# Optimization experiments

Hardware: AMD Instinct MI355X
Metric: run time of the kernel (lower is better)

The kernel has to match this reference:

```python
import jax, jax.numpy as jnp
import numpy as np

N = 100000
E = 3200000
D = 128


def setup_inputs() -> dict:
    key = jax.random.key(0)
    k1, k2, k3, k4 = jax.random.split(key, 4)
    x = jax.random.normal(k1, (N, D), dtype=jnp.float32)
    edge_index = jax.random.randint(k2, (2, E), 0, N, dtype=jnp.int64)
    W1 = jax.random.normal(k3, (D, 16), dtype=jnp.float32) * (1.0 / np.sqrt(D))
    b1 = jnp.zeros((16,), dtype=jnp.float32)
    W2 = jax.random.normal(k4, (16, 2), dtype=jnp.float32) * (1.0 / np.sqrt(16))
    b2 = jnp.zeros((2,), dtype=jnp.float32)
    return {"x": x, "edge_index": edge_index, "W1": W1, "b1": b1, "W2": W2, "b2": b2}


def _gcn_conv(h, src, dst, norm, W, b):
    # transform first (out_dim <= in_dim), then normalized scatter-add aggregation
    h = h @ W                                   # [N, out]
    msg = h[src] * norm[:, None]                # [E+N, out] gathered messages
    agg = jax.ops.segment_sum(msg, dst, num_segments=N)
    return agg + b


def reference(x, edge_index, W1, b1, W2, b2):
    loops = jnp.arange(N, dtype=edge_index.dtype)
    src = jnp.concatenate([edge_index[0], loops])   # row (message source)
    dst = jnp.concatenate([edge_index[1], loops])   # col (aggregation target)
    # symmetric GCN normalization: deg over dst, norm = d^-1/2[src] * d^-1/2[dst]
    deg = jax.ops.segment_sum(jnp.ones_like(src, dtype=x.dtype), dst, num_segments=N)
    dinv = jnp.where(deg > 0, jax.lax.rsqrt(deg), 0.0)
    norm = dinv[src] * dinv[dst]

    h = _gcn_conv(x, src, dst, norm, W1, b1)
    h = jax.nn.relu(h)
    h = _gcn_conv(h, src, dst, norm, W2, b2)
    return jax.nn.log_softmax(h, axis=1)
```

## Files before the change

kernel.cpp:

```cpp
#include <hip/hip_runtime.h>
#include <hip/hip_fp16.h>
#include <math.h>

#define N_NODES 100000
#define N_EDGES 3200000
#define D_IN    128
#define H1      16

#define BSH     8
#define NPB     256
#define NB      391
#define CAP     13056
#define PBLK    512
#define CHUNK   6250
#define ELS_CAP 12128
#define NLINES  (ELS_CAP / 16)
#define MROWS   64


__global__ __launch_bounds__(512) void k_zero(int* __restrict__ cursor) {
    int t = threadIdx.x;
    if (t < NB) cursor[t] = 0;
}

__global__ __launch_bounds__(512) void k_partition(const int* __restrict__ ei,
                                                   int* __restrict__ cursor,
                                                   unsigned int* __restrict__ eop) {
    __shared__ int h[512];
    __shared__ int loff[512];
    __shared__ int resv[NB];
    __shared__ unsigned short owner[NLINES];
    __shared__ unsigned char rank8[CHUNK];
    __shared__ unsigned int els[ELS_CAP];
    int t = threadIdx.x;
    h[t] = 0;
    __syncthreads();
    int c0 = blockIdx.x * CHUNK;
    const int* srcs = ei + c0;
    const int* dsts = ei + N_EDGES + c0;
    for (int i = t; i < CHUNK; i += 512)
        rank8[i] = (unsigned char)atomicAdd(&h[dsts[i] >> BSH], 1);
    __syncthreads();
    int cp = (h[t] + 15) & ~15;
    loff[t] = cp;
    __syncthreads();
    for (int o = 1; o < 512; o <<= 1) {
        int u = (t >= o) ? loff[t - o] : 0;
        __syncthreads();
        loff[t] += u;
        __syncthreads();
    }
    int inc = loff[t];
    int totalpad = loff[511];
    int ex = inc - cp;
    __syncthreads();
    loff[t] = ex;
    if (t < NB && cp) {
        resv[t] = atomicAdd(&cursor[t], cp);
        int l0 = ex >> 4;
        for (int k = 0; k < (cp >> 4); ++k) owner[l0 + k] = (unsigned short)t;
    }
    for (int i = t; i < totalpad; i += 512) els[i] = 0xFFFFFFFFu;
    __syncthreads();
    for (int i = t; i < CHUNK; i += 512) {
        int s = srcs[i];
        int d = dsts[i];
        int b = d >> BSH;
        els[loff[b] + (int)rank8[i]] = ((unsigned)s << BSH) | (unsigned)(d & (NPB - 1));
    }
    __syncthreads();
    for (int i = t; i < totalpad; i += 512) {
        int b   = owner[i >> 4];
        int pos = resv[b] + (i - loff[b]);
        if (pos < CAP)
            eop[(size_t)b * CAP + pos] = els[i];
    }
}

__global__ __launch_bounds__(512) void k_build(const int* __restrict__ cursor,
                                               unsigned int* __restrict__ eop,
                                               int* __restrict__ nstart,
                                               int* __restrict__ ndeg,
                                               float* __restrict__ dinv) {
    __shared__ unsigned int els[CAP];
    __shared__ int cnt[NPB];
    __shared__ int off[NPB];
    __shared__ int cur[NPB];
    int t = threadIdx.x, b = blockIdx.x;
    if (t < NPB) cnt[t] = 0;
    __syncthreads();
    int n = cursor[b]; if (n > CAP) n = CAP;
    unsigned int* reg = eop + (size_t)b * CAP;
    for (int i = t; i < n; i += 512) {
        unsigned int v = reg[i];
        els[i] = v;
        if ((int)v >= 0) atomicAdd(&cnt[v & (NPB - 1)], 1);
    }
    __syncthreads();
    int val = (t < NPB) ? cnt[t] : 0;
    if (t < NPB) off[t] = val;
    __syncthreads();
    for (int o = 1; o < NPB; o <<= 1) {
        int u = 0;
        if (t < NPB && t >= o) u = off[t - o];
        __syncthreads();
        if (t < NPB) off[t] += u;
        __syncthreads();
    }
    if (t < NPB) {
        int ex = off[t] - val;
        int node = (b << BSH) + t;
        if (node < N_NODES) {
            nstart[node] = b * CAP + ex;
            ndeg[node]   = val;
            dinv[node]   = rsqrtf((float)(val + 1));
        }
        cur[t] = ex;
    }
    __syncthreads();
    for (int i = t; i < n; i += 512) {
        unsigned int v = els[i];
        if ((int)v >= 0) {
            int r = atomicAdd(&cur[v & (NPB - 1)], 1);
            reg[r] = v >> BSH;
        }
    }
}

__global__ __launch_bounds__(256) void k_mm1(const float* __restrict__ x,
                                             const float* __restrict__ W1,
                                             const float* __restrict__ dinv,
                                             __half* __restrict__ h1h) {
    __shared__ float sX[MROWS][D_IN + 1];
    int t = threadIdx.x;
    int r0 = blockIdx.x * MROWS;
    for (int i = t; i < MROWS * (D_IN / 4); i += 256) {
        int row = i >> 5, c4 = i & 31;
        int grow = r0 + row;
        float4 v = (grow < N_NODES) ? ((const float4*)x)[(size_t)grow * 32 + c4]
                                    : make_float4(0.f, 0.f, 0.f, 0.f);
        sX[row][c4 * 4 + 0] = v.x; sX[row][c4 * 4 + 1] = v.y;
        sX[row][c4 * 4 + 2] = v.z; sX[row][c4 * 4 + 3] = v.w;
    }
    __syncthreads();
    int lane = t & 63;
    int c0 = __builtin_amdgcn_readfirstlane((t >> 6) * 4);
    float a0 = 0.f, a1 = 0.f, a2 = 0.f, a3 = 0.f;
#pragma unroll 4
    for (int d = 0; d < D_IN; ++d) {
        float xv = sX[lane][d];
        a0 = fmaf(xv, W1[d * 16 + c0 + 0], a0);
        a1 = fmaf(xv, W1[d * 16 + c0 + 1], a1);
        a2 = fmaf(xv, W1[d * 16 + c0 + 2], a2);
        a3 = fmaf(xv, W1[d * 16 + c0 + 3], a3);
    }
    int grow = r0 + lane;
    if (grow < N_NODES) {
        float di = dinv[grow];
        __half2* o = (__half2*)(h1h + (size_t)grow * H1 + c0);
        o[0] = __floats2half2_rn(a0 * di, a1 * di);
        o[1] = __floats2half2_rn(a2 * di, a3 * di);
    }
}

__global__ __launch_bounds__(256) void k_agg1(const unsigned int* __restrict__ eop,
                                              const int* __restrict__ nstart,
                                              const int* __restrict__ ndeg,
                                              const __half* __restrict__ h1h,
                                              const float* __restrict__ dinv,
                                              const float* __restrict__ b1,
                                              const float* __restrict__ W2,
                                              float2* __restrict__ h2f) {
    int t = threadIdx.x;
    int g = t >> 4, l = t & 15;
    int node = blockIdx.x * 16 + g;
    int e0 = nstart[node], e1 = e0 + ndeg[node];
    float acc = 0.f;
    int j = e0;
    for (; j + 4 <= e1; j += 4) {
        int s0 = eop[j], s1 = eop[j + 1], s2 = eop[j + 2], s3 = eop[j + 3];
        acc += __half2float(h1h[s0 * H1 + l]) + __half2float(h1h[s1 * H1 + l])
             + __half2float(h1h[s2 * H1 + l]) + __half2float(h1h[s3 * H1 + l]);
    }
    for (; j < e1; ++j) acc += __half2float(h1h[(int)eop[j] * H1 + l]);
    float di = dinv[node];
    float s  = acc + __half2float(h1h[node * H1 + l]);
    float h  = fmaxf(fmaf(di, s, b1[l]), 0.f);
    float p0 = h * W2[2 * l], p1 = h * W2[2 * l + 1];
#pragma unroll
    for (int off = 1; off < 16; off <<= 1) {
        p0 += __shfl_xor(p0, off);
        p1 += __shfl_xor(p1, off);
    }
    if (l == 0) h2f[node] = make_float2(p0 * di, p1 * di);
}

__global__ __launch_bounds__(256) void k_agg2(const unsigned int* __restrict__ eop,
                                              const int* __restrict__ nstart,
                                              const int* __restrict__ ndeg,
                                              const float2* __restrict__ h2f,
                                              const float* __restrict__ dinv,
                                              const float* __restrict__ b2,
                                              float* __restrict__ out) {
    int tg = blockIdx.x * 256 + threadIdx.x;
    int node = tg >> 2, l = tg & 3;
    if (node >= N_NODES) return;
    int e0 = nstart[node], e1 = e0 + ndeg[node];
    float ax = 0.f, ay = 0.f;
    for (int j = e0 + l; j < e1; j += 4) {
        float2 m = h2f[eop[j]];
        ax += m.x; ay += m.y;
    }
    ax += __shfl_xor(ax, 1); ay += __shfl_xor(ay, 1);
    ax += __shfl_xor(ax, 2); ay += __shfl_xor(ay, 2);
    if (l == 0) {
        float di = dinv[node];
        float2 self = h2f[node];
        float a0 = fmaf(di, ax + self.x, b2[0]);
        float a1 = fmaf(di, ay + self.y, b2[1]);
        float m  = fmaxf(a0, a1);
        float lg = logf(expf(a0 - m) + expf(a1 - m));
        out[2 * node]     = a0 - m - lg;
        out[2 * node + 1] = a1 - m - lg;
    }
}

extern "C" void kernel_launch(void* const* d_in, const int* in_sizes, int n_in,
                              void* d_out, int out_size, void* d_ws, size_t ws_size,
                              hipStream_t stream) {
    const float* x  = (const float*)d_in[0];
    const int*   ei = (const int*)d_in[1];
    const float* W1 = (const float*)d_in[2];
    const float* b1 = (const float*)d_in[3];
    const float* W2 = (const float*)d_in[4];
    const float* b2 = (const float*)d_in[5];
    float* out = (float*)d_out;

    int*          cursor = (int*)d_ws;
    int*          nstart = cursor + 512;
    int*          ndeg   = nstart + 100352;
    float*        dinv   = (float*)(ndeg + 100352);
    __half*       h1h    = (__half*)(dinv + 100352);
    float2*       h2f    = (float2*)(h1h + (size_t)100352 * H1);
    unsigned int* eop    = (unsigned int*)(h2f + 100352);

    k_zero     <<<1,    512, 0, stream>>>(cursor);
    k_partition<<<PBLK, 512, 0, stream>>>(ei, cursor, eop);
    k_build    <<<NB,   512, 0, stream>>>(cursor, eop, nstart, ndeg, dinv);
    k_mm1      <<<(N_NODES + MROWS - 1) / MROWS, 256, 0, stream>>>(x, W1, dinv, h1h);
    k_agg1     <<<N_NODES / 16, 256, 0, stream>>>(eop, nstart, ndeg, h1h, dinv, b1, W2, h2f);
    k_agg2     <<<(N_NODES * 4 + 255) / 256, 256, 0, stream>>>(eop, nstart, ndeg, h2f, dinv, b2, out);
}
```

Measured before the change: 222.6 us.

## Split k_build per bucket into two half-node blocks writing a separate CSR buffer

Each destination bucket is now handled by two blocks, each owning half of the 256 nodes. Each block reads the bucket's partitioned edges from global memory twice instead of staging them in a 52KB shared array, and writes sources into a new output buffer rather than in place. This doubles the block count, removes the large LDS footprint so occupancy can rise, and avoids the read/write race of in-place compaction. The cost is doubled global reads of the edge buckets and an extra workspace region. There is also a risk of overflow if one half receives more than CAP/2 edges.

```diff
diff --git a/kernel.cpp b/kernel.cpp
--- a/kernel.cpp
+++ b/kernel.cpp
@@ -11,6 +11,7 @@
 #define NPB     256
 #define NB      391
 #define CAP     13056
+#define HCAP    (CAP / 2)
 #define PBLK    512
 #define CHUNK   6250
 #define ELS_CAP 12128
@@ -78,51 +79,56 @@
 }
 
 __global__ __launch_bounds__(512) void k_build(const int* __restrict__ cursor,
-                                               unsigned int* __restrict__ eop,
+                                               const unsigned int* __restrict__ eop,
+                                               unsigned int* __restrict__ eos,
                                                int* __restrict__ nstart,
                                                int* __restrict__ ndeg,
                                                float* __restrict__ dinv) {
-    __shared__ unsigned int els[CAP];
-    __shared__ int cnt[NPB];
-    __shared__ int off[NPB];
-    __shared__ int cur[NPB];
-    int t = threadIdx.x, b = blockIdx.x;
-    if (t < NPB) cnt[t] = 0;
+    __shared__ int cnt[128], off[128], cur[128];
+    int t = threadIdx.x;
+    int b = blockIdx.x >> 1, hh = blockIdx.x & 1;
+    if (t < 128) cnt[t] = 0;
     __syncthreads();
     int n = cursor[b]; if (n > CAP) n = CAP;
-    unsigned int* reg = eop + (size_t)b * CAP;
+    const unsigned int* reg = eop + (size_t)b * CAP;
     for (int i = t; i < n; i += 512) {
         unsigned int v = reg[i];
-        els[i] = v;
-        if ((int)v >= 0) atomicAdd(&cnt[v & (NPB - 1)], 1);
-    }
-    __syncthreads();
-    int val = (t < NPB) ? cnt[t] : 0;
-    if (t < NPB) off[t] = val;
-    __syncthreads();
-    for (int o = 1; o < NPB; o <<= 1) {
+        if ((int)v >= 0) {
+            int dloc = v & (NPB - 1);
+            if ((dloc >> 7) == hh) atomicAdd(&cnt[dloc & 127], 1);
+        }
+    }
+    __syncthreads();
+    int val = (t < 128) ? cnt[t] : 0;
+    if (t < 128) off[t] = val;
+    __syncthreads();
+    for (int o = 1; o < 128; o <<= 1) {
         int u = 0;
-        if (t < NPB && t >= o) u = off[t - o];
-        __syncthreads();
-        if (t < NPB) off[t] += u;
-        __syncthreads();
-    }
-    if (t < NPB) {
+        if (t < 128 && t >= o) u = off[t - o];
+        __syncthreads();
+        if (t < 128) off[t] += u;
+        __syncthreads();
+    }
+    if (t < 128) {
         int ex = off[t] - val;
-        int node = (b << BSH) + t;
+        int node = (b << BSH) + (hh << 7) + t;
         if (node < N_NODES) {
-            nstart[node] = b * CAP + ex;
+            nstart[node] = b * CAP + hh * HCAP + ex;
             ndeg[node]   = val;
             dinv[node]   = rsqrtf((float)(val + 1));
         }
         cur[t] = ex;
     }
     __syncthreads();
+    unsigned int* oreg = eos + (size_t)b * CAP + (size_t)hh * HCAP;
     for (int i = t; i < n; i += 512) {
-        unsigned int v = els[i];
+        unsigned int v = reg[i];
         if ((int)v >= 0) {
-            int r = atomicAdd(&cur[v & (NPB - 1)], 1);
-            reg[r] = v >> BSH;
+            int dloc = v & (NPB - 1);
+            if ((dloc >> 7) == hh) {
+                int r = atomicAdd(&cur[dloc & 127], 1);
+                oreg[r] = v >> BSH;
+            }
         }
     }
 }
@@ -163,7 +169,7 @@
     }
 }
 
-__global__ __launch_bounds__(256) void k_agg1(const unsigned int* __restrict__ eop,
+__global__ __launch_bounds__(256) void k_agg1(const unsigned int* __restrict__ eos,
                                               const int* __restrict__ nstart,
                                               const int* __restrict__ ndeg,
                                               const __half* __restrict__ h1h,
@@ -178,11 +184,11 @@
     float acc = 0.f;
     int j = e0;
     for (; j + 4 <= e1; j += 4) {
-        int s0 = eop[j], s1 = eop[j + 1], s2 = eop[j + 2], s3 = eop[j + 3];
+        int s0 = eos[j], s1 = eos[j + 1], s2 = eos[j + 2], s3 = eos[j + 3];
         acc += __half2float(h1h[s0 * H1 + l]) + __half2float(h1h[s1 * H1 + l])
              + __half2float(h1h[s2 * H1 + l]) + __half2float(h1h[s3 * H1 + l]);
     }
-    for (; j < e1; ++j) acc += __half2float(h1h[(int)eop[j] * H1 + l]);
+    for (; j < e1; ++j) acc += __half2float(h1h[(int)eos[j] * H1 + l]);
     float di = dinv[node];
     float s  = acc + __half2float(h1h[node * H1 + l]);
     float h  = fmaxf(fmaf(di, s, b1[l]), 0.f);
@@ -195,7 +201,7 @@
     if (l == 0) h2f[node] = make_float2(p0 * di, p1 * di);
 }
 
-__global__ __launch_bounds__(256) void k_agg2(const unsigned int* __restrict__ eop,
+__global__ __launch_bounds__(256) void k_agg2(const unsigned int* __restrict__ eos,
                                               const int* __restrict__ nstart,
                                               const int* __restrict__ ndeg,
                                               const float2* __restrict__ h2f,
@@ -208,7 +214,7 @@
     int e0 = nstart[node], e1 = e0 + ndeg[node];
     float ax = 0.f, ay = 0.f;
     for (int j = e0 + l; j < e1; j += 4) {
-        float2 m = h2f[eop[j]];
+        float2 m = h2f[eos[j]];
         ax += m.x; ay += m.y;
     }
     ax += __shfl_xor(ax, 1); ay += __shfl_xor(ay, 1);
@@ -243,11 +249,12 @@
     __half*       h1h    = (__half*)(dinv + 100352);
     float2*       h2f    = (float2*)(h1h + (size_t)100352 * H1);
     unsigned int* eop    = (unsigned int*)(h2f + 100352);
+    unsigned int* eos    = eop + (size_t)NB * CAP;
 
     k_zero     <<<1,    512, 0, stream>>>(cursor);
     k_partition<<<PBLK, 512, 0, stream>>>(ei, cursor, eop);
-    k_build    <<<NB,   512, 0, stream>>>(cursor, eop, nstart, ndeg, dinv);
+    k_build    <<<NB * 2, 512, 0, stream>>>(cursor, eop, eos, nstart, ndeg, dinv);
     k_mm1      <<<(N_NODES + MROWS - 1) / MROWS, 256, 0, stream>>>(x, W1, dinv, h1h);
-    k_agg1     <<<N_NODES / 16, 256, 0, stream>>>(eop, nstart, ndeg, h1h, dinv, b1, W2, h2f);
-    k_agg2     <<<(N_NODES * 4 + 255) / 256, 256, 0, stream>>>(eop, nstart, ndeg, h2f, dinv, b2, out);
-}
+    k_agg1     <<<N_NODES / 16, 256, 0, stream>>>(eos, nstart, ndeg, h1h, dinv, b1, W2, h2f);
+    k_agg2     <<<(N_NODES * 4 + 255) / 256, 256, 0, stream>>>(eos, nstart, ndeg, h2f, dinv, b2, out);
+}
```

Measured after the change: 233.7 us. +5.0%, slower.
